# Kernel tuning notes

Hardware: AMD Instinct MI355X
Metric: run time of the kernel (lower is better)

## Reference

```python
import jax, jax.numpy as jnp
import numpy as np
import math

TEMPERATURE = 0.07
BASE_TEMPERATURE = 0.07
THRESH = 0.5          # fraction of class treated as positives (forward arg, static)
N_CLASSES = 64        # balanced batch: bsz % N_CLASSES == 0


def _quantile_sorted(v, t):
    """torch.quantile with 'linear' interpolation on an already-sorted last axis.
    t is a static Python float."""
    m = v.shape[-1]
    pos = t * (m - 1)
    i = int(math.floor(pos))
    frac = pos - i
    i2 = min(i + 1, m - 1)
    return v[..., i] * (1.0 - frac) + v[..., i2] * frac


def _supcon_loss(features, labels):
    bsz, n_views, d = features.shape
    T = TEMPERATURE
    # L2-normalize each view embedding (F.normalize, eps=1e-12)
    norm = jnp.maximum(jnp.linalg.norm(features, axis=2, keepdims=True), 1e-12)
    feats = features / norm
    # contrast_feature = cat(unbind(dim=1)) -> view-major stacking [V*bsz, d]
    contrast = jnp.transpose(feats, (1, 0, 2)).reshape(n_views * bsz, d)
    anchor = contrast                      # contrast_mode == 'all'
    N = n_views * bsz
    a_labels = jnp.tile(labels, n_views)   # labels.repeat(V)

    # scaled pairwise similarity [N, N]
    adc = jnp.matmul(anchor, contrast.T) / T
    logits = adc - jax.lax.stop_gradient(jnp.max(adc, axis=1, keepdims=True))

    same = (a_labels[:, None] == a_labels[None, :]).astype(feats.dtype)
    logits_mask = 1.0 - jnp.eye(N, dtype=feats.dtype)       # remove self
    mask = same * logits_mask
    aug_mask = jnp.tile(jnp.eye(bsz, dtype=feats.dtype), (n_views, n_views))

    # shift positives above zero so the m largest sorted entries per row are
    # exactly the non-augmentation positives
    temp = (adc + 2.0 / T) * mask * (1.0 - aug_mask)

    # balanced classes: every row has exactly m = V*(count-1) positives, so the
    # original per-class python loop (sort by label, slice segments, quantile)
    # reduces to one vectorized per-row quantile over the top-m sorted entries.
    count = bsz // N_CLASSES
    m = n_views * (count - 1)
    sorted_rows = jnp.sort(temp, axis=-1)[:, -m:]           # [N, m]

    q = 1.0 - THRESH
    lo_t = math.floor(m * q) / m
    hi_t = math.ceil(m * q) / m
    prob = m * q - math.floor(m * q)                        # 0.0 here (m*q integer)
    lo = _quantile_sorted(sorted_rows, lo_t)
    hi = _quantile_sorted(sorted_rows, hi_t)
    u = jax.random.uniform(jax.random.key(42), lo.shape)
    quant = jax.lax.stop_gradient(jnp.where(u < prob, hi, lo))  # [N]

    thr_mask = temp > quant[:, None]
    mask = mask * jnp.logical_or(thr_mask, aug_mask > 0).astype(feats.dtype)

    exp_logits = jnp.exp(logits) * logits_mask
    log_prob = logits - jnp.log(exp_logits.sum(axis=1, keepdims=True))
    mean_log_prob_pos = (mask * log_prob).sum(axis=1) / mask.sum(axis=1)
    loss = -(T / BASE_TEMPERATURE) * mean_log_prob_pos
    return loss.reshape(n_views, bsz).mean()


def setup_inputs() -> dict:
    key = jax.random.key(0)
    kf, _ = jax.random.split(key)
    bsz, n_views, d = 2048, 2, 512
    features = jax.random.normal(kf, (bsz, n_views, d), dtype=jnp.float32)
    # balanced labels: 64 classes x 32 samples (required by the vectorized
    # per-class quantile; matches a balanced-batch sampler)
    labels = (jnp.arange(bsz) % N_CLASSES).astype(jnp.int32)
    return {"features": features, "labels": labels}


def reference(features, labels):
    return _supcon_loss(features, labels)
```

## Files before the change

kernel.cpp:

```cpp
#include <hip/hip_runtime.h>
#include <hip/hip_bf16.h>

#define NTOT 4096
#define DIM  512
#define TILE 128
#define BK   32

constexpr float INV_T = 1.0f / 0.07f;

typedef short bf16x8 __attribute__((ext_vector_type(8)));
typedef float f32x4  __attribute__((ext_vector_type(4)));

__device__ __forceinline__ void gload16(const void* g, void* l) {
    __builtin_amdgcn_global_load_lds((const __attribute__((address_space(1))) void*)g,
                                     (__attribute__((address_space(3))) void*)l, 16, 0, 0);
}

__global__ __launch_bounds__(128) void k_norm(const float* __restrict__ feats,
                                              __hip_bfloat16* __restrict__ Zb,
                                              float* __restrict__ esum) {
    int row = blockIdx.x;
    int v = row >> 11, s = row & 2047;
    const float4* src = reinterpret_cast<const float4*>(feats + (size_t)(s * 2 + v) * DIM);
    int t = threadIdx.x;
    float4 x = src[t];
    float ss = x.x * x.x + x.y * x.y + x.z * x.z + x.w * x.w;
#pragma unroll
    for (int o = 32; o; o >>= 1) ss += __shfl_xor(ss, o);
    __shared__ float w2[2];
    if ((t & 63) == 0) w2[t >> 6] = ss;
    __syncthreads();
    float tot = w2[0] + w2[1];
    float sc = 1.0f / fmaxf(sqrtf(tot), 1e-12f);
    __hip_bfloat16 h[4];
    h[0] = __float2bfloat16(x.x * sc);
    h[1] = __float2bfloat16(x.y * sc);
    h[2] = __float2bfloat16(x.z * sc);
    h[3] = __float2bfloat16(x.w * sc);
    reinterpret_cast<ushort4*>(Zb + (size_t)row * DIM)[t] = *reinterpret_cast<ushort4*>(h);
    if (t == 0) esum[row] = 0.0f;
}

__global__ __launch_bounds__(256) void k_gemm(const __hip_bfloat16* __restrict__ Zb,
                                              float* __restrict__ posv,
                                              float* __restrict__ esum) {
    __shared__ __hip_bfloat16 lA[TILE * BK];
    __shared__ __hip_bfloat16 lB[TILE * BK];
    int t = threadIdx.x, lane = t & 63, wid = t >> 6;
    int ib = blockIdx.y, jb = blockIdx.x;
    int wr = wid >> 1, wc = wid & 1;

    f32x4 acc[4][4];
#pragma unroll
    for (int m = 0; m < 4; ++m)
#pragma unroll
        for (int n = 0; n < 4; ++n) acc[m][n] = (f32x4){0.f, 0.f, 0.f, 0.f};

    int c0 = wid * 64 + lane;
    int c1 = 256 + c0;
    const __hip_bfloat16* gA0 = Zb + (size_t)(ib * TILE + (c0 >> 2)) * DIM + (c0 & 3) * 8;
    const __hip_bfloat16* gA1 = Zb + (size_t)(ib * TILE + (c1 >> 2)) * DIM + (c1 & 3) * 8;
    const __hip_bfloat16* gB0 = Zb + (size_t)(jb * TILE + (c0 >> 2)) * DIM + (c0 & 3) * 8;
    const __hip_bfloat16* gB1 = Zb + (size_t)(jb * TILE + (c1 >> 2)) * DIM + (c1 & 3) * 8;
    __hip_bfloat16* lA0 = lA + (size_t)(wid * 64) * 8;
    __hip_bfloat16* lA1 = lA + (size_t)(256 + wid * 64) * 8;
    __hip_bfloat16* lB0 = lB + (size_t)(wid * 64) * 8;
    __hip_bfloat16* lB1 = lB + (size_t)(256 + wid * 64) * 8;

    const __hip_bfloat16* pa = lA + (size_t)(wr * 64 + (lane & 15)) * BK + (lane >> 4) * 8;
    const __hip_bfloat16* pb = lB + (size_t)(wc * 64 + (lane & 15)) * BK + (lane >> 4) * 8;

    for (int kt = 0; kt < DIM / BK; ++kt) {
        __syncthreads();
        gload16(gA0 + kt * BK, lA0);
        gload16(gA1 + kt * BK, lA1);
        gload16(gB0 + kt * BK, lB0);
        gload16(gB1 + kt * BK, lB1);
        __syncthreads();
        bf16x8 aF[4], bF[4];
#pragma unroll
        for (int m = 0; m < 4; ++m) aF[m] = *reinterpret_cast<const bf16x8*>(pa + m * 16 * BK);
#pragma unroll
        for (int n = 0; n < 4; ++n) bF[n] = *reinterpret_cast<const bf16x8*>(pb + n * 16 * BK);
#pragma unroll
        for (int m = 0; m < 4; ++m)
#pragma unroll
            for (int n = 0; n < 4; ++n)
                acc[m][n] = __builtin_amdgcn_mfma_f32_16x16x32_bf16(aF[m], bF[n], acc[m][n], 0, 0, 0);
    }

    int ibase = ib * TILE + wr * 64;
    int jbase = jb * TILE + wc * 64;
    float psum[4][4];
#pragma unroll
    for (int m = 0; m < 4; ++m)
#pragma unroll
        for (int r = 0; r < 4; ++r) psum[m][r] = 0.0f;

#pragma unroll
    for (int m = 0; m < 4; ++m) {
#pragma unroll
        for (int n = 0; n < 4; ++n) {
#pragma unroll
            for (int r = 0; r < 4; ++r) {
                int gi = ibase + m * 16 + (lane >> 4) * 4 + r;
                int gj = jbase + n * 16 + (lane & 15);
                float dv = acc[m][n][r];
                if (gj != gi) psum[m][r] += __expf((dv - 1.0f) * INV_T);
                if (((gj ^ gi) & 63) == 0) posv[((size_t)gi << 6) + (gj >> 6)] = dv;
            }
        }
    }
#pragma unroll
    for (int m = 0; m < 4; ++m) {
#pragma unroll
        for (int r = 0; r < 4; ++r) {
            float s = psum[m][r];
            s += __shfl_xor(s, 1);
            s += __shfl_xor(s, 2);
            s += __shfl_xor(s, 4);
            s += __shfl_xor(s, 8);
            if ((lane & 15) == 0)
                atomicAdd(&esum[ibase + m * 16 + (lane >> 4) * 4 + r], s);
        }
    }
}

__global__ __launch_bounds__(256) void k_loss(const float* __restrict__ posv,
                                              const float* __restrict__ esum,
                                              float* __restrict__ partials) {
    int t = threadIdx.x, wave = t >> 6, lane = t & 63;
    int row = blockIdx.x * 4 + wave;
    float v = posv[((size_t)row << 6) + lane];
    int self_slot = row >> 6;
    int aug_slot  = (row ^ 2048) >> 6;
    bool valid = (lane != self_slot) && (lane != aug_slot);
    float key = valid ? v : -1e30f;

    int rank = 0;
#pragma unroll
    for (int k = 0; k < 64; ++k) {
        float vk = __shfl(key, k);
        rank += (vk < key || (vk == key && k < lane)) ? 1 : 0;
    }
    float c30 = (rank == 32) ? key : -1e30f;
    float c31 = (rank == 33) ? key : -1e30f;
#pragma unroll
    for (int o = 32; o; o >>= 1) {
        c30 = fmaxf(c30, __shfl_xor(c30, o));
        c31 = fmaxf(c31, __shfl_xor(c31, o));
    }
    float qd = 0.5f * (c30 + c31);

    bool sel = valid && (key > qd);
    unsigned long long bal = __ballot(sel);
    int nsel = __popcll(bal);
    float contrib = sel ? (v - 1.0f) : 0.0f;
#pragma unroll
    for (int o = 32; o; o >>= 1) contrib += __shfl_xor(contrib, o);
    float vaug = __shfl(v, aug_slot);

    __shared__ float w4[4];
    if (lane == 0) {
        float total = (contrib + (vaug - 1.0f)) * INV_T;
        int cnt = nsel + 1;
        w4[wave] = total / (float)cnt - logf(esum[row]);
    }
    __syncthreads();
    if (t == 0) partials[blockIdx.x] = w4[0] + w4[1] + w4[2] + w4[3];
}

__global__ __launch_bounds__(256) void k_reduce(const float* __restrict__ partials,
                                                float* __restrict__ out) {
    int t = threadIdx.x;
    float s = partials[t] + partials[t + 256] + partials[t + 512] + partials[t + 768];
#pragma unroll
    for (int o = 32; o; o >>= 1) s += __shfl_xor(s, o);
    __shared__ float w4[4];
    if ((t & 63) == 0) w4[t >> 6] = s;
    __syncthreads();
    if (t == 0) *out = -(w4[0] + w4[1] + w4[2] + w4[3]) * (1.0f / (float)NTOT);
}

extern "C" void kernel_launch(void* const* d_in, const int* in_sizes, int n_in,
                              void* d_out, int out_size, void* d_ws, size_t ws_size,
                              hipStream_t stream) {
    const float* feats = (const float*)d_in[0];
    float* out = (float*)d_out;
    char* ws = (char*)d_ws;
    __hip_bfloat16* Zb = (__hip_bfloat16*)ws;
    float* posv = (float*)(ws + (size_t)NTOT * DIM * 2);
    float* esum = posv + (size_t)NTOT * 64;
    float* partials = esum + NTOT;

    k_norm<<<dim3(NTOT), dim3(128), 0, stream>>>(feats, Zb, esum);
    k_gemm<<<dim3(NTOT / TILE, NTOT / TILE), dim3(256), 0, stream>>>(Zb, posv, esum);
    k_loss<<<dim3(NTOT / 4), dim3(256), 0, stream>>>(posv, esum, partials);
    k_reduce<<<dim3(1), dim3(256), 0, stream>>>(partials, out);
}
```

Before: 107.2 us.

## Exploit Gram matrix symmetry: compute upper-triangular tiles only, add column sums

The similarity GEMM now launches only the upper-triangular tile blocks, 528 instead of 1024, and uses each off-diagonal tile for both its row and column exp-sums. The positive-pair values are written in both orientations, so roughly half of the MFMA work and global loads go away. The cost is extra column reductions and atomics per off-diagonal tile, plus a small triangular index decode. Separately, the normalization kernel now handles one row per wave, four rows per block, which removes the shared-memory reduction and the block barrier.

```diff
diff --git a/kernel.cpp b/kernel.cpp
--- a/kernel.cpp
+++ b/kernel.cpp
@@ -16,29 +16,29 @@
                                      (__attribute__((address_space(3))) void*)l, 16, 0, 0);
 }
 
-__global__ __launch_bounds__(128) void k_norm(const float* __restrict__ feats,
+__global__ __launch_bounds__(256) void k_norm(const float* __restrict__ feats,
                                               __hip_bfloat16* __restrict__ Zb,
                                               float* __restrict__ esum) {
-    int row = blockIdx.x;
+    int t = threadIdx.x, wave = t >> 6, lane = t & 63;
+    int row = blockIdx.x * 4 + wave;
     int v = row >> 11, s = row & 2047;
     const float4* src = reinterpret_cast<const float4*>(feats + (size_t)(s * 2 + v) * DIM);
-    int t = threadIdx.x;
-    float4 x = src[t];
-    float ss = x.x * x.x + x.y * x.y + x.z * x.z + x.w * x.w;
+    float4 x0 = src[lane];
+    float4 x1 = src[lane + 64];
+    float ss = x0.x*x0.x + x0.y*x0.y + x0.z*x0.z + x0.w*x0.w
+             + x1.x*x1.x + x1.y*x1.y + x1.z*x1.z + x1.w*x1.w;
 #pragma unroll
     for (int o = 32; o; o >>= 1) ss += __shfl_xor(ss, o);
-    __shared__ float w2[2];
-    if ((t & 63) == 0) w2[t >> 6] = ss;
-    __syncthreads();
-    float tot = w2[0] + w2[1];
-    float sc = 1.0f / fmaxf(sqrtf(tot), 1e-12f);
-    __hip_bfloat16 h[4];
-    h[0] = __float2bfloat16(x.x * sc);
-    h[1] = __float2bfloat16(x.y * sc);
-    h[2] = __float2bfloat16(x.z * sc);
-    h[3] = __float2bfloat16(x.w * sc);
-    reinterpret_cast<ushort4*>(Zb + (size_t)row * DIM)[t] = *reinterpret_cast<ushort4*>(h);
-    if (t == 0) esum[row] = 0.0f;
+    float sc = 1.0f / fmaxf(sqrtf(ss), 1e-12f);
+    __hip_bfloat16 h0[4], h1[4];
+    h0[0] = __float2bfloat16(x0.x * sc); h0[1] = __float2bfloat16(x0.y * sc);
+    h0[2] = __float2bfloat16(x0.z * sc); h0[3] = __float2bfloat16(x0.w * sc);
+    h1[0] = __float2bfloat16(x1.x * sc); h1[1] = __float2bfloat16(x1.y * sc);
+    h1[2] = __float2bfloat16(x1.z * sc); h1[3] = __float2bfloat16(x1.w * sc);
+    ushort4* dst = reinterpret_cast<ushort4*>(Zb + (size_t)row * DIM);
+    dst[lane]      = *reinterpret_cast<ushort4*>(h0);
+    dst[lane + 64] = *reinterpret_cast<ushort4*>(h1);
+    if (lane == 0) esum[row] = 0.0f;
 }
 
 __global__ __launch_bounds__(256) void k_gemm(const __hip_bfloat16* __restrict__ Zb,
@@ -47,7 +47,11 @@
     __shared__ __hip_bfloat16 lA[TILE * BK];
     __shared__ __hip_bfloat16 lB[TILE * BK];
     int t = threadIdx.x, lane = t & 63, wid = t >> 6;
-    int ib = blockIdx.y, jb = blockIdx.x;
+    int b = blockIdx.x;
+    int jb = (int)((sqrtf(8.0f * (float)b + 1.0f) - 1.0f) * 0.5f);
+    while ((jb + 1) * (jb + 2) / 2 <= b) ++jb;
+    while (jb * (jb + 1) / 2 > b) --jb;
+    int ib = b - jb * (jb + 1) / 2;
     int wr = wid >> 1, wc = wid & 1;
 
     f32x4 acc[4][4];
@@ -91,31 +95,57 @@
 
     int ibase = ib * TILE + wr * 64;
     int jbase = jb * TILE + wc * 64;
-    float psum[4][4];
+    float rsum[4][4];
 #pragma unroll
     for (int m = 0; m < 4; ++m)
 #pragma unroll
-        for (int r = 0; r < 4; ++r) psum[m][r] = 0.0f;
-
-#pragma unroll
-    for (int m = 0; m < 4; ++m) {
+        for (int r = 0; r < 4; ++r) rsum[m][r] = 0.0f;
+
+    if (ib == jb) {
+#pragma unroll
+        for (int m = 0; m < 4; ++m)
+#pragma unroll
+            for (int n = 0; n < 4; ++n)
+#pragma unroll
+                for (int r = 0; r < 4; ++r) {
+                    int gi = ibase + m * 16 + (lane >> 4) * 4 + r;
+                    int gj = jbase + n * 16 + (lane & 15);
+                    float dv = acc[m][n][r];
+                    if (gj != gi) rsum[m][r] += __expf((dv - 1.0f) * INV_T);
+                    if (((gj ^ gi) & 63) == 0) posv[((size_t)gi << 6) + (gj >> 6)] = dv;
+                }
+    } else {
+        float csum[4] = {0.f, 0.f, 0.f, 0.f};
+#pragma unroll
+        for (int m = 0; m < 4; ++m)
+#pragma unroll
+            for (int n = 0; n < 4; ++n)
+#pragma unroll
+                for (int r = 0; r < 4; ++r) {
+                    int gi = ibase + m * 16 + (lane >> 4) * 4 + r;
+                    int gj = jbase + n * 16 + (lane & 15);
+                    float dv = acc[m][n][r];
+                    float e = __expf((dv - 1.0f) * INV_T);
+                    rsum[m][r] += e;
+                    csum[n] += e;
+                    if (((gj ^ gi) & 63) == 0) {
+                        posv[((size_t)gi << 6) + (gj >> 6)] = dv;
+                        posv[((size_t)gj << 6) + (gi >> 6)] = dv;
+                    }
+                }
 #pragma unroll
         for (int n = 0; n < 4; ++n) {
-#pragma unroll
-            for (int r = 0; r < 4; ++r) {
-                int gi = ibase + m * 16 + (lane >> 4) * 4 + r;
-                int gj = jbase + n * 16 + (lane & 15);
-                float dv = acc[m][n][r];
-                if (gj != gi) psum[m][r] += __expf((dv - 1.0f) * INV_T);
-                if (((gj ^ gi) & 63) == 0) posv[((size_t)gi << 6) + (gj >> 6)] = dv;
-            }
+            float s = csum[n];
+            s += __shfl_xor(s, 16);
+            s += __shfl_xor(s, 32);
+            if (lane < 16) atomicAdd(&esum[jbase + n * 16 + lane], s);
         }
     }
 #pragma unroll
-    for (int m = 0; m < 4; ++m) {
+    for (int m = 0; m < 4; ++m)
 #pragma unroll
         for (int r = 0; r < 4; ++r) {
-            float s = psum[m][r];
+            float s = rsum[m][r];
             s += __shfl_xor(s, 1);
             s += __shfl_xor(s, 2);
             s += __shfl_xor(s, 4);
@@ -123,7 +153,6 @@
             if ((lane & 15) == 0)
                 atomicAdd(&esum[ibase + m * 16 + (lane >> 4) * 4 + r], s);
         }
-    }
 }
 
 __global__ __launch_bounds__(256) void k_loss(const float* __restrict__ posv,
@@ -193,8 +222,9 @@
     float* esum = posv + (size_t)NTOT * 64;
     float* partials = esum + NTOT;
 
-    k_norm<<<dim3(NTOT), dim3(128), 0, stream>>>(feats, Zb, esum);
-    k_gemm<<<dim3(NTOT / TILE, NTOT / TILE), dim3(256), 0, stream>>>(Zb, posv, esum);
+    const int NTILE = NTOT / TILE;
+    k_norm<<<dim3(NTOT / 4), dim3(256), 0, stream>>>(feats, Zb, esum);
+    k_gemm<<<dim3(NTILE * (NTILE + 1) / 2), dim3(256), 0, stream>>>(Zb, posv, esum);
     k_loss<<<dim3(NTOT / 4), dim3(256), 0, stream>>>(posv, esum, partials);
     k_reduce<<<dim3(1), dim3(256), 0, stream>>>(partials, out);
 }
```

Measured after the change: 101.8 us. 1.05x faster.
